# Optimization experiments

Measured on AMD Instinct MI355X. Metric: run time of the kernel, lower is better.

## Reference

```python
import jax, jax.numpy as jnp
import numpy as np

NEG_INF = -jnp.inf
BIG_NEG = -1.0e9


def setup_inputs() -> dict:
    key = jax.random.key(0)
    ks = jax.random.split(key, 8)
    B, S, H = 8, 2048, 1024
    x = jax.random.normal(ks[0], (B, S, H), dtype=jnp.float32)
    attention_mask = jax.random.randint(ks[1], (B, S), 0, 2).astype(jnp.bool_)
    # keep first token always valid so no row is fully padded by the pad mask
    attention_mask = attention_mask.at[:, 0].set(True)
    scale = 0.02
    Wq = jax.random.normal(ks[2], (H, H), dtype=jnp.float32) * scale
    bq = jax.random.normal(ks[3], (H,), dtype=jnp.float32) * scale
    Wk = jax.random.normal(ks[4], (H, H), dtype=jnp.float32) * scale
    bk = jax.random.normal(ks[5], (H,), dtype=jnp.float32) * scale
    Wv = jax.random.normal(ks[6], (H, H), dtype=jnp.float32) * scale
    bv = jax.random.normal(ks[7], (H,), dtype=jnp.float32) * scale
    return {"x": x, "attention_mask": attention_mask, "Wq": Wq, "bq": bq,
            "Wk": Wk, "bk": bk, "Wv": Wv, "bv": bv}


def reference(x, attention_mask, Wq, bq, Wk, bk, Wv, bv):
    H = x.shape[-1]
    scale = jnp.sqrt(jnp.float32(H))
    # torch.nn.Linear: x @ W.T + b
    Q = jnp.einsum('bsh,oh->bso', x, Wq) + bq
    K = jnp.einsum('bsh,oh->bso', x, Wk) + bk
    V = jnp.einsum('bsh,oh->bso', x, Wv) + bv
    scores = jnp.einsum('bqh,bkh->bqk', Q, K) / scale  # [B,S,S]
    # faithful to masked_fill(tril(scores)==0, -inf): masks upper triangle
    # AND any lower-triangle score that is exactly zero
    scores = jnp.where(jnp.tril(scores) == 0, NEG_INF, scores)
    pad = attention_mask[:, :, None] & attention_mask[:, None, :]  # [B,S,S]
    scores = jnp.where(pad, scores, NEG_INF)
    # replace -inf with -1e9 (fully-masked rows -> uniform softmax, as in torch)
    scores = jnp.where(jnp.isneginf(scores), BIG_NEG, scores)
    attn = jax.nn.softmax(scores, axis=-1)
    return jnp.einsum('bqk,bkh->bqh', attn, V)
```

## Files before the change

kernel.cpp:

```cpp
#include <hip/hip_runtime.h>
#include <stdint.h>

typedef __bf16 bf16x8 __attribute__((ext_vector_type(8)));
typedef float f32x4 __attribute__((ext_vector_type(4)));

#define BB 8
#define SS 2048
#define HH 1024

#define TILE_B   32768ll
#define NTRI     136
#define BATCH_B  (NTRI * TILE_B)

#define OFF_Q      0ll
#define OFF_K      33554432ll
#define OFF_VT     67108864ll
#define OFF_MASK   100663296ll
#define OFF_MEANV  100679680ll
#define OFF_VIDX   100712448ll
#define OFF_CIDX   100777984ll
#define OFF_NV     100843520ll
#define OFF_TMP    101711872ll
#define OFF_XBF    (OFF_TMP)
#define OFF_WBF    (OFF_TMP + 33554432ll)
#define OFF_VTC    (OFF_TMP)
#define OFF_SCORES (OFF_TMP + 33554432ll)

__device__ __forceinline__ unsigned short f2bf(float f) {
  unsigned int u = __float_as_uint(f);
  u += 0x7FFFu + ((u >> 16) & 1u);
  return (unsigned short)(u >> 16);
}
__device__ __forceinline__ float bf2f(unsigned short u) {
  return __uint_as_float(((unsigned int)u) << 16);
}

__device__ __forceinline__ void gl_lds16(const void* g, void* l) {
  __builtin_amdgcn_global_load_lds(
      (const __attribute__((address_space(1))) void*)g,
      (__attribute__((address_space(3))) void*)l, 16, 0, 0);
}

__global__ __launch_bounds__(1024) void canon_mask(
    const unsigned char* __restrict__ m, unsigned char* __restrict__ out) {
  __shared__ int cnt[4];
  const int t = threadIdx.x;
  if (t < 4) cnt[t] = 0;
  __syncthreads();
  uint4 v = ((const uint4*)m)[t];
  const unsigned char* pb = (const unsigned char*)&v;
  int loc[4] = {0, 0, 0, 0};
#pragma unroll
  for (int j = 0; j < 16; ++j)
    if (pb[j]) loc[j & 3]++;
#pragma unroll
  for (int r = 0; r < 4; ++r)
    if (loc[r]) atomicAdd(&cnt[r], loc[r]);
  __syncthreads();
  const int c0 = cnt[0], c1 = cnt[1], c2 = cnt[2], c3 = cnt[3];
  unsigned char ob[16];
  if (c0 > 0 && c1 == 0 && c2 == 0 && c3 == 0) {
    const int* mi = (const int*)m;
#pragma unroll
    for (int j = 0; j < 16; ++j) ob[j] = mi[t * 16 + j] ? 1 : 0;
  } else if (c0 == 0 && (c2 > 0 || c3 > 0)) {
    const float* mf = (const float*)m;
#pragma unroll
    for (int j = 0; j < 16; ++j) ob[j] = (mf[t * 16 + j] != 0.0f) ? 1 : 0;
  } else {
#pragma unroll
    for (int j = 0; j < 16; ++j) ob[j] = pb[j] ? 1 : 0;
  }
  ((uint4*)out)[t] = *(const uint4*)ob;
}

__global__ __launch_bounds__(256) void build_compact(
    const unsigned char* __restrict__ mask, int* __restrict__ vidx,
    int* __restrict__ cidx, int* __restrict__ nv) {
  const int b = blockIdx.x;
  const int t = threadIdx.x;
  __shared__ int cnt[256];
  __shared__ int totalS;
  const unsigned char* mb = mask + b * SS;
  unsigned char m[8];
  int c = 0;
#pragma unroll
  for (int j = 0; j < 8; ++j) { m[j] = mb[t * 8 + j]; c += m[j] ? 1 : 0; }
  cnt[t] = c;
  __syncthreads();
  int base = 0;
  for (int i = 0; i < t; ++i) base += cnt[i];
  if (t == 255) totalS = base + c;
  int pos = base;
  int* vb = vidx + b * SS;
  int* cb = cidx + b * SS;
#pragma unroll
  for (int j = 0; j < 8; ++j) {
    const int s = t * 8 + j;
    if (m[j]) { vb[pos] = s; cb[s] = pos; ++pos; }
    else cb[s] = -1;
  }
  __syncthreads();
  const int total = totalS;
  if (t == 0) nv[b] = total;
  for (int idx = total + t; idx < SS; idx += 256) vb[idx] = 0;
}

__global__ void cvt_f32_bf16(const float* __restrict__ in,
                             unsigned short* __restrict__ out, int n4) {
  int i = blockIdx.x * blockDim.x + threadIdx.x;
  int stride = gridDim.x * blockDim.x;
  for (; i < n4; i += stride) {
    float4 v = ((const float4*)in)[i];
    ushort4 o;
    o.x = f2bf(v.x); o.y = f2bf(v.y); o.z = f2bf(v.z); o.w = f2bf(v.w);
    ((ushort4*)out)[i] = o;
  }
}

__global__ void cvt_w3(const float* __restrict__ Wq, const float* __restrict__ Wk,
                       const float* __restrict__ Wv, unsigned short* __restrict__ out) {
  const int z = blockIdx.y;
  const float* src = (z == 0) ? Wq : (z == 1) ? Wk : Wv;
  unsigned short* dst = out + (long)z * (HH * HH);
  const int n4 = HH * HH / 4;
  int i = blockIdx.x * 256 + threadIdx.x;
  for (; i < n4; i += 256 * 256) {
    float4 v = ((const float4*)src)[i];
    ushort4 o;
    o.x = f2bf(v.x); o.y = f2bf(v.y); o.z = f2bf(v.z); o.w = f2bf(v.w);
    ((ushort4*)dst)[i] = o;
  }
}

__global__ __launch_bounds__(256) void vtc_gather(
    const unsigned short* __restrict__ Vt, const int* __restrict__ vidx,
    const int* __restrict__ nv, unsigned short* __restrict__ Vtc) {
  const int h = blockIdx.x;
  const int b = blockIdx.y;
  const int t = threadIdx.x;
  const unsigned short* src = Vt + ((long)b * HH + h) * SS;
  unsigned short* dst = Vtc + ((long)b * HH + h) * SS;
  const int n = nv[b];
  const int* vb = vidx + b * SS;
  const int j0 = t * 8;
  unsigned short o[8];
#pragma unroll
  for (int k = 0; k < 8; ++k) {
    const int j = j0 + k;
    o[k] = (j < n) ? src[vb[j]] : (unsigned short)0;
  }
  *(ushort4*)(dst + j0) = *(const ushort4*)o;
  *(ushort4*)(dst + j0 + 4) = *(const ushort4*)(o + 4);
}

__global__ __launch_bounds__(256) void fixup_masked(
    float* __restrict__ out, const unsigned char* __restrict__ mask,
    const float* __restrict__ sums) {
  const long row = blockIdx.x;
  if (mask[row]) return;
  const long b = row >> 11;
  const int t = threadIdx.x;
  float4 v = ((const float4*)(sums + b * HH))[t];
  v.x *= (1.f / 2048.f); v.y *= (1.f / 2048.f);
  v.z *= (1.f / 2048.f); v.w *= (1.f / 2048.f);
  ((float4*)(out + row * HH))[t] = v;
}

__global__ __launch_bounds__(512, 2) void gemm256(
    const unsigned short* __restrict__ Abase,
    const unsigned short* __restrict__ Bbase, long bStride,
    char* __restrict__ Cq, char* __restrict__ Ck, char* __restrict__ VtOut,
    const float* __restrict__ biasq, const float* __restrict__ biask,
    const float* __restrict__ biasv, float* __restrict__ meanV,
    const int* __restrict__ cidxg) {
  extern __shared__ char smem[];
  const int tid = threadIdx.x;
  const int wave = tid >> 6, lane = tid & 63;
  const int wr = wave >> 2, wc = wave & 3;
  const int l15 = lane & 15, l4 = lane >> 4;
  const int bz = blockIdx.z;
  const int bm = blockIdx.x, bn = blockIdx.y;

  const char* A = (const char*)Abase;
  const char* B = (const char*)(Bbase + (long)bz * bStride);

  const int srow = tid >> 3;
  const int gslot = (tid & 7) ^ (srow & 7);
  const char* gA = A + ((long)bm * 256 + srow) * 2048 + gslot * 16;
  const char* gB = B + ((long)bn * 256 + srow) * 2048 + gslot * 16;
  const int ldsStageW = wave << 10;

#define STG(kt_, type_, buf_) do { \
    const char* _g = (((type_) < 2) ? gA : gB) + \
                     (((type_) & 1) ? 262144 : 0) + ((long)(kt_) << 7); \
    char* _l = smem + ((buf_) << 16) + (((type_) >> 1) << 15) + \
               (((type_) & 1) << 14) + ldsStageW; \
    gl_lds16(_g, _l); \
    gl_lds16(_g + 131072, _l + 8192); } while (0)

  const int sw0 = ((l4 ^ (l15 & 7)) << 4);
  const int sw1 = (((4 + l4) ^ (l15 & 7)) << 4);
  const int aB0 = (wr << 14) + l15 * 128 + sw0;
  const int aB1 = (wr << 14) + l15 * 128 + sw1;
  const int bB0 = 32768 + ((wc >> 1) << 14) + (((wc & 1) << 6) + l15) * 128 + sw0;
  const int bB1 = 32768 + ((wc >> 1) << 14) + (((wc & 1) << 6) + l15) * 128 + sw1;

  f32x4 acc[8][4];
  const f32x4 z4 = {0.f, 0.f, 0.f, 0.f};
#pragma unroll
  for (int m = 0; m < 8; ++m)
#pragma unroll
    for (int n = 0; n < 4; ++n) acc[m][n] = z4;

  STG(0, 0, 0); STG(0, 1, 0); STG(0, 2, 0); STG(0, 3, 0);
  STG(1, 0, 1); STG(1, 1, 1); STG(1, 2, 1); STG(1, 3, 1);
  asm volatile("s_waitcnt vmcnt(8)" ::: "memory");
  __builtin_amdgcn_s_barrier();
  __builtin_amdgcn_sched_barrier(0);

  bf16x8 aC[4][2], bLo[2][2], bHi[2][2];

  for (int it = 0; it < 8; ++it) {
#pragma unroll
    for (int g = 0; g < 8; ++g) {
      const int buf = (g < 4) ? 0 : 65536;
      const int q = g & 3;
      if (q == 0) {
#pragma unroll
        for (int mm = 0; mm < 4; ++mm) {
          aC[mm][0] = *(const bf16x8*)(smem + buf + aB0 + mm * 2048);
          aC[mm][1] = *(const bf16x8*)(smem + buf + aB1 + mm * 2048);
        }
#pragma unroll
        for (int nn = 0; nn < 2; ++nn) {
          bLo[nn][0] = *(const bf16x8*)(smem + buf + bB0 + nn * 2048);
          bLo[nn][1] = *(const bf16x8*)(smem + buf + bB1 + nn * 2048);
        }
      } else if (q == 1) {
#pragma unroll
        for (int nn = 0; nn < 2; ++nn) {
          bHi[nn][0] = *(const bf16x8*)(smem + buf + bB0 + (2 + nn) * 2048);
          bHi[nn][1] = *(const bf16x8*)(smem + buf + bB1 + (2 + nn) * 2048);
        }
      } else if (q == 2) {
#pragma unroll
        for (int mm = 0; mm < 4; ++mm) {
          aC[mm][0] = *(const bf16x8*)(smem + buf + aB0 + (4 + mm) * 2048);
          aC[mm][1] = *(const bf16x8*)(smem + buf + aB1 + (4 + mm) * 2048);
        }
      }
      {
        const int u = it * 8 + g - 2;
        if (u >= 0) {
          const int kt = 2 + (u >> 2);
          if (kt < 16) {
            if (g == 0)      STG(kt, 0, 1);
            else if (g == 1) STG(kt, 1, 1);
            else if (g == 2) STG(kt, 2, 0);
            else if (g == 3) STG(kt, 3, 0);
            else if (g == 4) STG(kt, 0, 0);
            else if (g == 5) STG(kt, 1, 0);
            else if (g == 6) STG(kt, 2, 1);
            else             STG(kt, 3, 1);
          }
        }
      }
      __builtin_amdgcn_s_barrier();
      asm volatile("s_waitcnt lgkmcnt(0)" ::: "memory");
      __builtin_amdgcn_sched_barrier(0);
      __builtin_amdgcn_s_setprio(1);
      if (q == 0) {
#pragma unroll
        for (int mm = 0; mm < 4; ++mm)
#pragma unroll
          for (int nn = 0; nn < 2; ++nn) {
            acc[mm][nn] = __builtin_amdgcn_mfma_f32_16x16x32_bf16(
                aC[mm][0], bLo[nn][0], acc[mm][nn], 0, 0, 0);
            acc[mm][nn] = __builtin_amdgcn_mfma_f32_16x16x32_bf16(
                aC[mm][1], bLo[nn][1], acc[mm][nn], 0, 0, 0);
          }
      } else if (q == 1) {
#pragma unroll
        for (int mm = 0; mm < 4; ++mm)
#pragma unroll
          for (int nn = 0; nn < 2; ++nn) {
            acc[mm][2 + nn] = __builtin_amdgcn_mfma_f32_16x16x32_bf16(
                aC[mm][0], bHi[nn][0], acc[mm][2 + nn], 0, 0, 0);
            acc[mm][2 + nn] = __builtin_amdgcn_mfma_f32_16x16x32_bf16(
                aC[mm][1], bHi[nn][1], acc[mm][2 + nn], 0, 0, 0);
          }
      } else if (q == 2) {
#pragma unroll
        for (int mm = 0; mm < 4; ++mm)
#pragma unroll
          for (int nn = 0; nn < 2; ++nn) {
            acc[4 + mm][2 + nn] = __builtin_amdgcn_mfma_f32_16x16x32_bf16(
                aC[mm][0], bHi[nn][0], acc[4 + mm][2 + nn], 0, 0, 0);
            acc[4 + mm][2 + nn] = __builtin_amdgcn_mfma_f32_16x16x32_bf16(
                aC[mm][1], bHi[nn][1], acc[4 + mm][2 + nn], 0, 0, 0);
          }
      } else {
#pragma unroll
        for (int mm = 0; mm < 4; ++mm)
#pragma unroll
          for (int nn = 0; nn < 2; ++nn) {
            acc[4 + mm][nn] = __builtin_amdgcn_mfma_f32_16x16x32_bf16(
                aC[mm][0], bLo[nn][0], acc[4 + mm][nn], 0, 0, 0);
            acc[4 + mm][nn] = __builtin_amdgcn_mfma_f32_16x16x32_bf16(
                aC[mm][1], bLo[nn][1], acc[4 + mm][nn], 0, 0, 0);
          }
      }
      __builtin_amdgcn_s_setprio(0);
      __builtin_amdgcn_sched_barrier(0);
      if (q == 3) {
        if (g == 3 && it == 7)
          asm volatile("s_waitcnt vmcnt(0)" ::: "memory");
        else
          asm volatile("s_waitcnt vmcnt(4)" ::: "memory");
      }
      __builtin_amdgcn_s_barrier();
      asm volatile("" ::: "memory");
    }
  }
#undef STG

  const int rl0 = (wr << 7) + (l4 << 2);
  const int cl0 = (wc << 6) + l15;

  if (bz < 2) {
    const float* bias = (bz == 0) ? biasq : biask;
#pragma unroll
    for (int n = 0; n < 4; ++n) {
      const int cl = cl0 + n * 16;
      const float bv = bias[bn * 256 + cl];
      const int colx = cl ^ (l4 << 4);
#pragma unroll
      for (int m = 0; m < 8; ++m) {
        const int rl = rl0 + m * 16;
#pragma unroll
        for (int r = 0; r < 4; ++r)
          *(unsigned short*)(smem + (rl + r) * 512 + colx * 2) =
              f2bf(acc[m][n][r] + bv);
      }
    }
    __syncthreads();
    unsigned short* C = (unsigned short*)((bz == 0) ? Cq : Ck);
    const int rowg0 = bm * 256;
    const long colb0 = (long)bn * 512;
#pragma unroll
    for (int i = 0; i < 16; ++i) {
      const int s2 = i * 512 + tid;
      const int row = s2 >> 5;
      const int cb = s2 & 31;
      const int lb = (row * 512 + (cb << 4)) ^ (((row >> 2) & 3) << 5);
      const int grow = rowg0 + row;
      const int cr = cidxg[grow];
      if (cr >= 0)
        *(uint4*)((char*)C + ((long)(grow >> 11) * 2048 + cr) * 2048 +
                  colb0 + (cb << 4)) = *(const uint4*)(smem + lb);
    }
  } else {
#pragma unroll
    for (int n = 0; n < 4; ++n) {
      const int h = cl0 + n * 16;
      const float bv = biasv[bn * 256 + h];
      const int xr = (h & 7) << 4;
#pragma unroll
      for (int m = 0; m < 8; ++m) {
        const int s0a = rl0 + m * 16;
        uint2 w;
        w.x = (unsigned)f2bf(acc[m][n][0] + bv) |
              ((unsigned)f2bf(acc[m][n][1] + bv) << 16);
        w.y = (unsigned)f2bf(acc[m][n][2] + bv) |
              ((unsigned)f2bf(acc[m][n][3] + bv) << 16);
        *(uint2*)(smem + h * 512 + ((s0a * 2) ^ xr)) = w;
      }
    }
    __syncthreads();
    char* VtB = VtOut + (long)(bm >> 3) * (SS * HH * 2) + (long)(bm & 7) * 512;
#pragma unroll
    for (int i = 0; i < 16; ++i) {
      const int s2 = i * 512 + tid;
      const int h = s2 >> 5;
      const int cb = s2 & 31;
      const int lb = h * 512 + ((cb << 4) ^ ((h & 7) << 4));
      *(uint4*)(VtB + (long)(bn * 256 + h) * 4096 + cb * 16) =
          *(const uint4*)(smem + lb);
    }
    float* mv = meanV + (long)(bm >> 3) * HH + (long)bn * 256;
#pragma unroll
    for (int n = 0; n < 4; ++n) {
      const int h = cl0 + n * 16;
      float s = 32.0f * biasv[bn * 256 + h];
#pragma unroll
      for (int m = 0; m < 8; ++m)
        s += acc[m][n][0] + acc[m][n][1] + acc[m][n][2] + acc[m][n][3];
      atomicAdd(&mv[h], s);
    }
  }
}

__global__ __launch_bounds__(256, 2) void gemm128s(
    const unsigned short* __restrict__ Qc, const unsigned short* __restrict__ Kc,
    char* __restrict__ scoresBase, const int* __restrict__ nv) {
  __shared__ __align__(16) char smem[65536];
  const int tid = threadIdx.x;
  const int wave = tid >> 6, lane = tid & 63;
  const int wr = wave >> 1, wc = wave & 1;
  const int l15 = lane & 15, l4 = lane >> 4;
  const int bz = blockIdx.y;

  int t0 = blockIdx.x, bm = 0, a_ = 0;
  while (a_ + bm + 1 <= t0) { ++bm; a_ += bm; }
  const int bn = t0 - a_;

  const int nt = (nv[bz] + 127) >> 7;
  if (bm >= nt) return;

  const unsigned short* A = Qc + (long)bz * SS * HH;
  const unsigned short* B = Kc + (long)bz * SS * HH;

  const int s0 = tid, s1 = tid + 256;
  const int rA0 = ((s0 >> 3) << 1) | (((s0 >> 2) & 1) ^ ((s0 >> 4) & 1));
  const int cA0 = (s0 & 3) ^ (rA0 & 3);
  const int rA1 = ((s1 >> 3) << 1) | (((s1 >> 2) & 1) ^ ((s1 >> 4) & 1));
  const int cA1 = (s1 & 3) ^ (rA1 & 3);
  const char* aG0 = (const char*)A + (long)(bm * 128 + rA0) * 2048 + cA0 * 16;
  const char* aG1 = (const char*)A + (long)(bm * 128 + rA1) * 2048 + cA1 * 16;
  const char* bG0 = (const char*)B + (long)(bn * 128 + rA0) * 2048 + cA0 * 16;
  const char* bG1 = (const char*)B + (long)(bn * 128 + rA1) * 2048 + cA1 * 16;
  const int ldsL0 = wave << 10;
  const int ldsL1 = 4096 + (wave << 10);

#define STG(t_) do { \
    char* _p = smem + (((t_) & 3) << 14); \
    const long _ko = (long)(t_) << 6; \
    gl_lds16(aG0 + _ko, _p + ldsL0); \
    gl_lds16(aG1 + _ko, _p + ldsL1); \
    gl_lds16(bG0 + _ko, _p + 8192 + ldsL0); \
    gl_lds16(bG1 + _ko, _p + 8192 + ldsL1); } while (0)

  const int baseSwz = ((l15 * 64 + (l4 << 4)) ^ ((l15 & 7) << 4));
  const int rdA = (wr << 12) + baseSwz;
  const int rdB = 8192 + (wc << 12) + baseSwz;

  f32x4 acc[4][4];
  const f32x4 z4 = {0.f, 0.f, 0.f, 0.f};
#pragma unroll
  for (int m = 0; m < 4; ++m)
#pragma unroll
    for (int n = 0; n < 4; ++n) acc[m][n] = z4;

  STG(0); STG(1); STG(2);
  asm volatile("s_waitcnt vmcnt(8)" ::: "memory");
  __builtin_amdgcn_s_barrier();
  __builtin_amdgcn_sched_barrier(0);

  const int kT = 32;
  for (int t = 0; t < kT; ++t) {
    if (t + 3 < kT) STG(t + 3);
    const char* bufp = smem + ((t & 3) << 14);
    bf16x8 af[4], bg[4];
#pragma unroll
    for (int m = 0; m < 4; ++m)
      af[m] = *(const bf16x8*)(bufp + rdA + (m << 10));
#pragma unroll
    for (int n = 0; n < 4; ++n)
      bg[n] = *(const bf16x8*)(bufp + rdB + (n << 10));
    __builtin_amdgcn_s_setprio(1);
#pragma unroll
    for (int m = 0; m < 4; ++m)
#pragma unroll
      for (int n = 0; n < 4; ++n)
        acc[m][n] = __builtin_amdgcn_mfma_f32_16x16x32_bf16(af[m], bg[n],
                                                            acc[m][n], 0, 0, 0);
    __builtin_amdgcn_s_setprio(0);
    __builtin_amdgcn_sched_barrier(0);
    if (t + 3 < kT)       asm volatile("s_waitcnt vmcnt(8)" ::: "memory");
    else if (t + 3 == kT) asm volatile("s_waitcnt vmcnt(4)" ::: "memory");
    else if (t + 2 == kT) asm volatile("s_waitcnt vmcnt(0)" ::: "memory");
    if (t + 1 < kT) {
      __builtin_amdgcn_s_barrier();
      __builtin_amdgcn_sched_barrier(0);
      asm volatile("" ::: "memory");
    }
  }
#undef STG

  const int rl0 = (wr << 6) + (l4 << 2);
  const int cl0 = (wc << 6) + l15;
  char* Ct = scoresBase + (long)bz * BATCH_B + (long)t0 * TILE_B;
  __syncthreads();
#pragma unroll
  for (int m = 0; m < 4; ++m)
#pragma unroll
    for (int r = 0; r < 4; ++r) {
      const int ql = rl0 + m * 16 + r;
      const int qg = bm * 128 + ql;
#pragma unroll
      for (int n = 0; n < 4; ++n) {
        const int kg = bn * 128 + cl0 + n * 16;
        const float v = (kg <= qg) ? acc[m][n][r] * 0.03125f : -1.0e9f;
        const int colx = (cl0 + n * 16) ^ (l4 << 4);
        *(unsigned short*)(smem + ql * 256 + colx * 2) = f2bf(v);
      }
    }
  __syncthreads();
#pragma unroll
  for (int i = 0; i < 8; ++i) {
    const int s2 = i * 256 + tid;
    const int row = s2 >> 4;
    const int cb = s2 & 15;
    const int lb = row * 256 + ((cb << 4) ^ (((row >> 2) & 3) << 5));
    *(uint4*)(Ct + (long)row * 256 + (cb << 4)) = *(const uint4*)(smem + lb);
  }
}

__global__ __launch_bounds__(256) void softmax_tri(char* __restrict__ base,
                                                   const int* __restrict__ nv) {
  const int r = blockIdx.x;
  const int bz = blockIdx.y;
  if (r >= nv[bz]) return;
  const int bm = r >> 7;
  const int w = (bm + 1) << 7;
  char* bb = base + (long)bz * BATCH_B +
             (long)(bm * (bm + 1) / 2) * TILE_B + (long)(r & 127) * 256;
  const int t = threadIdx.x;
  const bool act = (t << 3) < w;
  const int bn = t >> 4;
  const int cl = (t << 3) & 127;
  char* slot = bb + (long)bn * TILE_B + (long)cl * 2;
  float v[8];
  float m = -3.0e38f;
  if (act) {
    ushort4 u0 = ((const ushort4*)slot)[0];
    ushort4 u1 = ((const ushort4*)slot)[1];
    v[0] = bf2f(u0.x); v[1] = bf2f(u0.y); v[2] = bf2f(u0.z); v[3] = bf2f(u0.w);
    v[4] = bf2f(u1.x); v[5] = bf2f(u1.y); v[6] = bf2f(u1.z); v[7] = bf2f(u1.w);
#pragma unroll
    for (int k = 0; k < 8; ++k) m = fmaxf(m, v[k]);
  }
  __shared__ float red[8];
#pragma unroll
  for (int off = 32; off > 0; off >>= 1) m = fmaxf(m, __shfl_down(m, off, 64));
  const int wid = t >> 6, lane = t & 63;
  if (lane == 0) red[wid] = m;
  __syncthreads();
  m = fmaxf(fmaxf(red[0], red[1]), fmaxf(red[2], red[3]));
  float e[8];
  float s = 0.f;
  if (act) {
#pragma unroll
    for (int k = 0; k < 8; ++k) { e[k] = __expf(v[k] - m); s += e[k]; }
  }
#pragma unroll
  for (int off = 32; off > 0; off >>= 1) s += __shfl_down(s, off, 64);
  if (lane == 0) red[4 + wid] = s;
  __syncthreads();
  s = red[4] + red[5] + red[6] + red[7];
  const float inv = 1.0f / s;
  if (act) {
    ushort4 o0, o1;
    o0.x = f2bf(e[0] * inv); o0.y = f2bf(e[1] * inv);
    o0.z = f2bf(e[2] * inv); o0.w = f2bf(e[3] * inv);
    o1.x = f2bf(e[4] * inv); o1.y = f2bf(e[5] * inv);
    o1.z = f2bf(e[6] * inv); o1.w = f2bf(e[7] * inv);
    ((ushort4*)slot)[0] = o0;
    ((ushort4*)slot)[1] = o1;
  }
}

__global__ __launch_bounds__(256, 2) void gemm_pv(
    const char* __restrict__ attn, const unsigned short* __restrict__ Vtc,
    float* __restrict__ Out, const int* __restrict__ vidx,
    const int* __restrict__ nv) {
  __shared__ __align__(16) char smem[65536];
  const int tid = threadIdx.x;
  const int wave = tid >> 6, lane = tid & 63;
  const int wr = wave >> 1, wc = wave & 1;
  const int l15 = lane & 15, l4 = lane >> 4;
  const int bz = blockIdx.z;
  const int bm = 15 - blockIdx.x;
  const int bn = blockIdx.y;

  const int nvb = nv[bz];
  const int nt = (nvb + 127) >> 7;
  if (bm >= nt) return;

  const char* Ab = attn + (long)bz * BATCH_B + (long)(bm * (bm + 1) / 2) * TILE_B;
  const unsigned short* B = Vtc + (long)bz * SS * HH;

  const int s0 = tid, s1 = tid + 256;
  const int rA0 = ((s0 >> 3) << 1) | (((s0 >> 2) & 1) ^ ((s0 >> 4) & 1));
  const int cA0 = (s0 & 3) ^ (rA0 & 3);
  const int rA1 = ((s1 >> 3) << 1) | (((s1 >> 2) & 1) ^ ((s1 >> 4) & 1));
  const int cA1 = (s1 & 3) ^ (rA1 & 3);
  const char* aB0 = Ab + (long)rA0 * 256 + cA0 * 16;
  const char* aB1 = Ab + (long)rA1 * 256 + cA1 * 16;
  const char* bG0 = (const char*)(B + (long)(bn * 128 + rA0) * SS) + cA0 * 16;
  const char* bG1 = (const char*)(B + (long)(bn * 128 + rA1) * SS) + cA1 * 16;
  const int ldsL0 = wave << 10;
  const int ldsL1 = 4096 + (wave << 10);

#define STGPV(t_) do { \
    char* _p = smem + (((t_) & 3) << 14); \
    const long _aO = (long)((t_) >> 2) * TILE_B + (long)((t_) & 3) * 64; \
    const long _bO = (long)(t_) << 6; \
    gl_lds16(aB0 + _aO, _p + ldsL0); \
    gl_lds16(aB1 + _aO, _p + ldsL1); \
    gl_lds16(bG0 + _bO, _p + 8192 + ldsL0); \
    gl_lds16(bG1 + _bO, _p + 8192 + ldsL1); } while (0)

  const int baseSwz = ((l15 * 64 + (l4 << 4)) ^ ((l15 & 7) << 4));
  const int rdA = (wr << 12) + baseSwz;
  const int rdB = 8192 + (wc << 12) + baseSwz;

  f32x4 acc[4][4];
  const f32x4 z4 = {0.f, 0.f, 0.f, 0.f};
#pragma unroll
  for (int m = 0; m < 4; ++m)
#pragma unroll
    for (int n = 0; n < 4; ++n) acc[m][n] = z4;

  STGPV(0); STGPV(1); STGPV(2);
  asm volatile("s_waitcnt vmcnt(8)" ::: "memory");
  __builtin_amdgcn_s_barrier();
  __builtin_amdgcn_sched_barrier(0);

  const int kT = (bm + 1) * 4;
  for (int t = 0; t < kT; ++t) {
    if (t + 3 < kT) STGPV(t + 3);
    const char* bufp = smem + ((t & 3) << 14);
    bf16x8 af[4], bg[4];
#pragma unroll
    for (int m = 0; m < 4; ++m)
      af[m] = *(const bf16x8*)(bufp + rdA + (m << 10));
#pragma unroll
    for (int n = 0; n < 4; ++n)
      bg[n] = *(const bf16x8*)(bufp + rdB + (n << 10));
    __builtin_amdgcn_s_setprio(1);
#pragma unroll
    for (int m = 0; m < 4; ++m)
#pragma unroll
      for (int n = 0; n < 4; ++n)
        acc[m][n] = __builtin_amdgcn_mfma_f32_16x16x32_bf16(af[m], bg[n],
                                                            acc[m][n], 0, 0, 0);
    __builtin_amdgcn_s_setprio(0);
    __builtin_amdgcn_sched_barrier(0);
    if (t + 3 < kT)       asm volatile("s_waitcnt vmcnt(8)" ::: "memory");
    else if (t + 3 == kT) asm volatile("s_waitcnt vmcnt(4)" ::: "memory");
    else if (t + 2 == kT) asm volatile("s_waitcnt vmcnt(0)" ::: "memory");
    if (t + 1 < kT) {
      __builtin_amdgcn_s_barrier();
      __builtin_amdgcn_sched_barrier(0);
      asm volatile("" ::: "memory");
    }
  }
#undef STGPV

  const int rl0 = (wr << 6) + (l4 << 2);
  const int cl0 = (wc << 6) + l15;
  __syncthreads();
#pragma unroll
  for (int m = 0; m < 4; ++m)
#pragma unroll
    for (int r = 0; r < 4; ++r) {
      const int ql = rl0 + m * 16 + r;
#pragma unroll
      for (int n = 0; n < 4; ++n) {
        const int colx = (cl0 + n * 16) ^ (l4 << 4);
        *(float*)(smem + ql * 512 + colx * 4) = acc[m][n][r];
      }
    }
  __syncthreads();
  const int* vb = vidx + (long)bz * SS;
#pragma unroll
  for (int i = 0; i < 16; ++i) {
    const int s2 = i * 256 + tid;
    const int row = s2 >> 5;
    const int cb = s2 & 31;
    const int lb = (row * 512 + (cb << 4)) ^ (((row >> 2) & 3) << 6);
    const int crow = bm * 128 + row;
    if (crow < nvb) {
      const int orig = vb[crow];
      *(uint4*)((char*)Out + (((long)bz * SS + orig) * HH) * 4 +
                (long)bn * 512 + (cb << 4)) = *(const uint4*)(smem + lb);
    }
  }
}

extern "C" void kernel_launch(void* const* d_in, const int* in_sizes, int n_in,
                              void* d_out, int out_size, void* d_ws, size_t ws_size,
                              hipStream_t stream) {
  (void)in_sizes; (void)n_in; (void)out_size; (void)ws_size;
  const float* x = (const float*)d_in[0];
  const unsigned char* mask_raw = (const unsigned char*)d_in[1];
  const float* Wq = (const float*)d_in[2];
  const float* bq = (const float*)d_in[3];
  const float* Wk = (const float*)d_in[4];
  const float* bk = (const float*)d_in[5];
  const float* Wv = (const float*)d_in[6];
  const float* bv = (const float*)d_in[7];
  char* ws = (char*)d_ws;

  unsigned short* Xbf = (unsigned short*)(ws + OFF_XBF);
  unsigned short* Wbf = (unsigned short*)(ws + OFF_WBF);
  unsigned short* Qc = (unsigned short*)(ws + OFF_Q);
  unsigned short* Kc = (unsigned short*)(ws + OFF_K);
  unsigned short* Vt = (unsigned short*)(ws + OFF_VT);
  unsigned short* Vtc = (unsigned short*)(ws + OFF_VTC);
  unsigned char* mask = (unsigned char*)(ws + OFF_MASK);
  float* meanV = (float*)(ws + OFF_MEANV);
  int* vidx = (int*)(ws + OFF_VIDX);
  int* cidx = (int*)(ws + OFF_CIDX);
  int* nv = (int*)(ws + OFF_NV);

  const long MS = (long)BB * SS;

  (void)hipFuncSetAttribute((const void*)gemm256,
                            hipFuncAttributeMaxDynamicSharedMemorySize, 131072);

  canon_mask<<<1, 1024, 0, stream>>>(mask_raw, mask);
  build_compact<<<BB, 256, 0, stream>>>(mask, vidx, cidx, nv);
  hipMemsetAsync(meanV, 0, (size_t)BB * HH * 4, stream);

  cvt_f32_bf16<<<2048, 256, 0, stream>>>(x, Xbf, (int)(MS * HH / 4));
  cvt_w3<<<dim3(256, 3), 256, 0, stream>>>(Wq, Wk, Wv, Wbf);

  gemm256<<<dim3(MS / 256, HH / 256, 3), 512, 131072, stream>>>(
      Xbf, Wbf, (long)HH * HH,
      (char*)Qc, (char*)Kc, (char*)Vt, bq, bk, bv, meanV, cidx);

  vtc_gather<<<dim3(HH, BB), 256, 0, stream>>>(Vt, vidx, nv, Vtc);

  gemm128s<<<dim3(NTRI, BB), 256, 0, stream>>>(
      Qc, Kc, ws + OFF_SCORES, nv);

  softmax_tri<<<dim3(SS, BB), 256, 0, stream>>>(ws + OFF_SCORES, nv);

  gemm_pv<<<dim3(SS / 128, HH / 128, BB), 256, 0, stream>>>(
      ws + OFF_SCORES, Vtc, (float*)d_out, vidx, nv);

  fixup_masked<<<BB * SS, 256, 0, stream>>>((float*)d_out, mask, meanV);
}
```

Before: 269.6 us.

## Gather valid rows in QK projection and skip fully padded row tiles

```diff
diff --git a/kernel.cpp b/kernel.cpp
--- a/kernel.cpp
+++ b/kernel.cpp
@@ -18,7 +18,6 @@
 #define OFF_MASK   100663296ll
 #define OFF_MEANV  100679680ll
 #define OFF_VIDX   100712448ll
-#define OFF_CIDX   100777984ll
 #define OFF_NV     100843520ll
 #define OFF_TMP    101711872ll
 #define OFF_XBF    (OFF_TMP)
@@ -76,7 +75,7 @@
 
 __global__ __launch_bounds__(256) void build_compact(
     const unsigned char* __restrict__ mask, int* __restrict__ vidx,
-    int* __restrict__ cidx, int* __restrict__ nv) {
+    int* __restrict__ nv) {
   const int b = blockIdx.x;
   const int t = threadIdx.x;
   __shared__ int cnt[256];
@@ -93,12 +92,10 @@
   if (t == 255) totalS = base + c;
   int pos = base;
   int* vb = vidx + b * SS;
-  int* cb = cidx + b * SS;
 #pragma unroll
   for (int j = 0; j < 8; ++j) {
     const int s = t * 8 + j;
-    if (m[j]) { vb[pos] = s; cb[s] = pos; ++pos; }
-    else cb[s] = -1;
+    if (m[j]) { vb[pos] = s; ++pos; }
   }
   __syncthreads();
   const int total = totalS;
@@ -173,7 +170,7 @@
     char* __restrict__ Cq, char* __restrict__ Ck, char* __restrict__ VtOut,
     const float* __restrict__ biasq, const float* __restrict__ biask,
     const float* __restrict__ biasv, float* __restrict__ meanV,
-    const int* __restrict__ cidxg) {
+    const int* __restrict__ vidx, const int* __restrict__ nv) {
   extern __shared__ char smem[];
   const int tid = threadIdx.x;
   const int wave = tid >> 6, lane = tid & 63;
@@ -182,22 +179,36 @@
   const int bz = blockIdx.z;
   const int bm = blockIdx.x, bn = blockIdx.y;
 
-  const char* A = (const char*)Abase;
+  const int b = bm >> 3;
+  const int rInB = (bm & 7) * 256;
+  if (bz < 2 && rInB >= nv[b]) return;
+
   const char* B = (const char*)(Bbase + (long)bz * bStride);
 
   const int srow = tid >> 3;
   const int gslot = (tid & 7) ^ (srow & 7);
-  const char* gA = A + ((long)bm * 256 + srow) * 2048 + gslot * 16;
+  const int* vb = vidx + b * SS;
+  const char* aS[4];
+#pragma unroll
+  for (int j = 0; j < 4; ++j) {
+    const int r = rInB + srow + 64 * j;
+    const int vr = (bz < 2) ? vb[r] : r;
+    aS[j] = (const char*)Abase + ((long)b * SS + vr) * 2048 + gslot * 16;
+  }
   const char* gB = B + ((long)bn * 256 + srow) * 2048 + gslot * 16;
   const int ldsStageW = wave << 10;
 
 #define STG(kt_, type_, buf_) do { \
-    const char* _g = (((type_) < 2) ? gA : gB) + \
-                     (((type_) & 1) ? 262144 : 0) + ((long)(kt_) << 7); \
     char* _l = smem + ((buf_) << 16) + (((type_) >> 1) << 15) + \
                (((type_) & 1) << 14) + ldsStageW; \
-    gl_lds16(_g, _l); \
-    gl_lds16(_g + 131072, _l + 8192); } while (0)
+    if ((type_) < 2) { \
+      gl_lds16(aS[(type_) * 2]     + ((long)(kt_) << 7), _l); \
+      gl_lds16(aS[(type_) * 2 + 1] + ((long)(kt_) << 7), _l + 8192); \
+    } else { \
+      const char* _g = gB + (((type_) & 1) ? 262144 : 0) + ((long)(kt_) << 7); \
+      gl_lds16(_g, _l); \
+      gl_lds16(_g + 131072, _l + 8192); \
+    } } while (0)
 
   const int sw0 = ((l4 ^ (l15 & 7)) << 4);
   const int sw1 = (((4 + l4) ^ (l15 & 7)) << 4);
@@ -346,7 +357,7 @@
     }
     __syncthreads();
     unsigned short* C = (unsigned short*)((bz == 0) ? Cq : Ck);
-    const int rowg0 = bm * 256;
+    const long rowg0 = (long)b * SS + rInB;
     const long colb0 = (long)bn * 512;
 #pragma unroll
     for (int i = 0; i < 16; ++i) {
@@ -354,11 +365,8 @@
       const int row = s2 >> 5;
       const int cb = s2 & 31;
       const int lb = (row * 512 + (cb << 4)) ^ (((row >> 2) & 3) << 5);
-      const int grow = rowg0 + row;
-      const int cr = cidxg[grow];
-      if (cr >= 0)
-        *(uint4*)((char*)C + ((long)(grow >> 11) * 2048 + cr) * 2048 +
-                  colb0 + (cb << 4)) = *(const uint4*)(smem + lb);
+      *(uint4*)((char*)C + (rowg0 + row) * 2048 + colb0 + (cb << 4)) =
+          *(const uint4*)(smem + lb);
     }
   } else {
 #pragma unroll
@@ -378,7 +386,7 @@
       }
     }
     __syncthreads();
-    char* VtB = VtOut + (long)(bm >> 3) * (SS * HH * 2) + (long)(bm & 7) * 512;
+    char* VtB = VtOut + (long)b * (SS * HH * 2) + (long)(bm & 7) * 512;
 #pragma unroll
     for (int i = 0; i < 16; ++i) {
       const int s2 = i * 512 + tid;
@@ -388,7 +396,7 @@
       *(uint4*)(VtB + (long)(bn * 256 + h) * 4096 + cb * 16) =
           *(const uint4*)(smem + lb);
     }
-    float* mv = meanV + (long)(bm >> 3) * HH + (long)bn * 256;
+    float* mv = meanV + (long)b * HH + (long)bn * 256;
 #pragma unroll
     for (int n = 0; n < 4; ++n) {
       const int h = cl0 + n * 16;
@@ -713,7 +721,6 @@
   unsigned char* mask = (unsigned char*)(ws + OFF_MASK);
   float* meanV = (float*)(ws + OFF_MEANV);
   int* vidx = (int*)(ws + OFF_VIDX);
-  int* cidx = (int*)(ws + OFF_CIDX);
   int* nv = (int*)(ws + OFF_NV);
 
   const long MS = (long)BB * SS;
@@ -722,7 +729,7 @@
                             hipFuncAttributeMaxDynamicSharedMemorySize, 131072);
 
   canon_mask<<<1, 1024, 0, stream>>>(mask_raw, mask);
-  build_compact<<<BB, 256, 0, stream>>>(mask, vidx, cidx, nv);
+  build_compact<<<BB, 256, 0, stream>>>(mask, vidx, nv);
   hipMemsetAsync(meanV, 0, (size_t)BB * HH * 4, stream);
 
   cvt_f32_bf16<<<2048, 256, 0, stream>>>(x, Xbf, (int)(MS * HH / 4));
@@ -730,7 +737,7 @@
 
   gemm256<<<dim3(MS / 256, HH / 256, 3), 512, 131072, stream>>>(
       Xbf, Wbf, (long)HH * HH,
-      (char*)Qc, (char*)Kc, (char*)Vt, bq, bk, bv, meanV, cidx);
+      (char*)Qc, (char*)Kc, (char*)Vt, bq, bk, bv, meanV, vidx, nv);
 
   vtc_gather<<<dim3(HH, BB), 256, 0, stream>>>(Vt, vidx, nv, Vtc);
 
```

Result: faster. 260.5 us (-3.4%).
